# Optimization experiments

Hardware: AMD Instinct MI355X
Metric: run time of the kernel (lower is better)

## Reference

```python
import jax, jax.numpy as jnp
import numpy as np
import math

B, T, N, D = 8, 12, 1000, 256
H, R = 8, 32
HD = D // H
E = 4 * D  # SwiGLU expansion


def setup_inputs() -> dict:
    key = jax.random.key(0)
    ks = jax.random.split(key, 12)
    s = 0.02
    return {
        "x": jax.random.normal(ks[0], (B, T, N, D), jnp.float32),
        "z": jax.random.normal(ks[1], (B, T, N, D), jnp.float32),
        # block params
        "norm1_w": jnp.ones((D,), jnp.float32),
        "norm2_w": jnp.ones((D,), jnp.float32),
        "alpha": jnp.float32(math.log(9)),
        "beta": jnp.float32(math.log(math.sqrt(2) + 1)),
        "gamma": jnp.float32(math.log(9)),
        "delta": jnp.float32(math.log(math.sqrt(2) + 1)),
        # low-rank attention params (Linear stored as [in, out])
        "Wq": jax.random.normal(ks[2], (D, D), jnp.float32) * s,
        "bq": jnp.zeros((D,), jnp.float32),
        "key_param": jax.random.normal(ks[3], (R, H, HD), jnp.float32),
        "Wv": jax.random.normal(ks[4], (D, D), jnp.float32) * s,
        "bv": jnp.zeros((D,), jnp.float32),
        "mha_alpha": jnp.full((H, 1), math.log(9), jnp.float32),
        "mha_beta": jnp.full((H, 1), math.log(0.01), jnp.float32),
        # SwiGLU FFN params
        "W1": jax.random.normal(ks[5], (D, E), jnp.float32) * s,
        "b1": jnp.zeros((E,), jnp.float32),
        "W2": jax.random.normal(ks[6], (D, E), jnp.float32) * s,
        "b2": jnp.zeros((E,), jnp.float32),
        "W3": jax.random.normal(ks[7], (E, D), jnp.float32) * s,
        "b3": jnp.zeros((D,), jnp.float32),
    }


def _rms_norm(x, w, eps=1e-6):
    return w * (x * jax.lax.rsqrt(jnp.mean(x * x, axis=-1, keepdims=True) + eps))


def reference(x, z, norm1_w, norm2_w, alpha, beta, gamma, delta,
              Wq, bq, key_param, Wv, bv, mha_alpha, mha_beta,
              W1, b1, W2, b2, W3, b3):
    sig = jax.nn.sigmoid
    x1 = _rms_norm(x, norm1_w)
    z1 = _rms_norm(sig(gamma) * x1 + sig(delta) * z, norm2_w)

    # SwiGLU FFN (dropout is identity in eval)
    ffn = (jax.nn.silu(x1 @ W1 + b1) * (x1 @ W2 + b2)) @ W3 + b3

    # Low-rank spatial attention
    q = (z1 @ Wq + bq).reshape(B, T, N, H, HD)
    attn = jnp.einsum('btnhd,rhd->btnhr', q, key_param) / jnp.float32(HD) ** 0.5
    xv = (x1 @ Wv + bv).reshape(B, T, N, H, HD)
    v = jnp.einsum('btnhr,btnhd->btrhd', jax.nn.softmax(attn, axis=-1), xv)
    v = jnp.einsum('btnhr,btrhd->btnhd', jax.nn.softmax(attn, axis=2), v)
    v = sig(mha_alpha) * xv + sig(mha_beta) * v  # (H,1) broadcasts over (h,d)
    mha = v.reshape(B, T, N, D)

    return sig(alpha) * ffn + sig(beta) * mha
```

## Files before the change

### kernel.cpp

```cpp
#include <hip/hip_runtime.h>
#include <math.h>

#define MT 96000
#define DD 256
#define EE 1024
#define NBT 96
#define NSEQ 1000

typedef __attribute__((ext_vector_type(8))) short bf16x8;
typedef __attribute__((ext_vector_type(4))) short bf16x4;
typedef __attribute__((ext_vector_type(4))) float f32x4;

__device__ __forceinline__ short f2b(float f) {
  union { float f; unsigned u; } v; v.f = f;
  unsigned r = (v.u + 0x7FFFu + ((v.u >> 16) & 1u)) >> 16;
  return (short)r;
}
__device__ __forceinline__ float b2f(short s) {
  union { unsigned u; float f; } v; v.u = ((unsigned)(unsigned short)s) << 16;
  return v.f;
}
__device__ __forceinline__ float sigf(float x) { return 1.f / (1.f + __expf(-x)); }
__device__ __forceinline__ f32x4 mfma16(bf16x8 a, bf16x8 b, f32x4 c) {
  return __builtin_amdgcn_mfma_f32_16x16x32_bf16(a, b, c, 0, 0, 0);
}
__device__ __forceinline__ unsigned cvtpk(float lo, float hi) {
  unsigned r;
  asm("v_cvt_pk_bf16_f32 %0, %1, %2" : "=v"(r) : "v"(lo), "v"(hi));
  return r;
}
__device__ __forceinline__ void gl_lds16(const short* gp, short* lp) {
  __builtin_amdgcn_global_load_lds(
      (const __attribute__((address_space(1))) void*)gp,
      (__attribute__((address_space(3))) void*)lp, 16, 0, 0);
}

__global__ __launch_bounds__(256) void k_prep(
    const float* __restrict__ Wq, const float* __restrict__ bq,
    const float* __restrict__ key, const float* __restrict__ Wv,
    const float* __restrict__ W1, const float* __restrict__ W2,
    const float* __restrict__ W3,
    short* __restrict__ W1t, short* __restrict__ W2t, short* __restrict__ W3t,
    short* __restrict__ Wvt, short* __restrict__ Wqkt, float* __restrict__ bqk)
{
  int i = blockIdx.x * 256 + threadIdx.x;
  { int e = i >> 8, c = i & 255;
    W1t[i] = f2b(W1[c * EE + e]);
    W2t[i] = f2b(W2[c * EE + e]); }
  { int n = i >> 10, e = i & 1023;
    W3t[i] = f2b(W3[e * DD + n]); }
  if (i < 65536) {
    int n = i >> 8, c = i & 255;
    Wvt[i] = f2b(Wv[c * DD + n]);
    int h = n >> 5, r = n & 31;
    float acc = 0.f;
    for (int d = 0; d < 32; ++d)
      acc += Wq[c * DD + h * 32 + d] * key[(r * 8 + h) * 32 + d];
    Wqkt[i] = f2b(acc * 0.17677669529663687f);
  }
  if (i < 256) {
    int h = i >> 5, r = i & 31;
    float acc = 0.f;
    for (int d = 0; d < 32; ++d)
      acc += bq[h * 32 + d] * key[(r * 8 + h) * 32 + d];
    bqk[i] = acc * 0.17677669529663687f;
  }
}

__global__ __launch_bounds__(256) void k_norm(
    const float* __restrict__ x, const float* __restrict__ z,
    const float* __restrict__ nw1, const float* __restrict__ nw2,
    const float* __restrict__ gamma, const float* __restrict__ delta,
    short* __restrict__ x1bp, short* __restrict__ z1bp)
{
  int tok = blockIdx.x * 4 + (threadIdx.x >> 6);
  int lane = threadIdx.x & 63;
  size_t rbase = (size_t)tok * DD;
  float4 xv = ((const float4*)(x + rbase))[lane];
  float ss = xv.x*xv.x + xv.y*xv.y + xv.z*xv.z + xv.w*xv.w;
  #pragma unroll
  for (int mm = 1; mm < 64; mm <<= 1) ss += __shfl_xor(ss, mm);
  float inv = rsqrtf(ss * 0.00390625f + 1e-6f);
  float4 wv = ((const float4*)nw1)[lane];
  float xa = xv.x * inv * wv.x, xb = xv.y * inv * wv.y,
        xc = xv.z * inv * wv.z, xd = xv.w * inv * wv.w;
  bf16x4 xo = { f2b(xa), f2b(xb), f2b(xc), f2b(xd) };
  ((bf16x4*)(x1bp + rbase))[lane] = xo;
  float sg = sigf(gamma[0]), sd = sigf(delta[0]);
  float4 zv = ((const float4*)(z + rbase))[lane];
  float t0 = sg*xa + sd*zv.x, t1 = sg*xb + sd*zv.y,
        t2 = sg*xc + sd*zv.z, t3 = sg*xd + sd*zv.w;
  float s2 = t0*t0 + t1*t1 + t2*t2 + t3*t3;
  #pragma unroll
  for (int mm = 1; mm < 64; mm <<= 1) s2 += __shfl_xor(s2, mm);
  float inv2 = rsqrtf(s2 * 0.00390625f + 1e-6f);
  float4 w2v = ((const float4*)nw2)[lane];
  bf16x4 zo = { f2b(t0*inv2*w2v.x), f2b(t1*inv2*w2v.y),
                f2b(t2*inv2*w2v.z), f2b(t3*inv2*w2v.w) };
  ((bf16x4*)(z1bp + rbase))[lane] = zo;
}

__global__ __launch_bounds__(256) void k_gemm256(
    const short* __restrict__ A, const short* __restrict__ Bt,
    const float* __restrict__ bias, short* __restrict__ C)
{
  __shared__ __align__(16) short As[64 * 40];
  __shared__ __align__(16) short Bs[64 * 40];
  int row0 = blockIdx.x * 64, col0 = blockIdx.y * 64;
  int tid = threadIdx.x, lane = tid & 63, w = tid >> 6;
  int mh = (w & 1) * 32, nh = (w >> 1) * 32;
  int l15 = lane & 15, ko = (lane >> 4) * 8;
  int lrow = tid >> 2, lch = (tid & 3) * 8;
  f32x4 acc[2][2] = {};
  for (int k0 = 0; k0 < 256; k0 += 32) {
    *(bf16x8*)&As[lrow * 40 + lch] = *(const bf16x8*)&A[(row0 + lrow) * 256 + k0 + lch];
    *(bf16x8*)&Bs[lrow * 40 + lch] = *(const bf16x8*)&Bt[(col0 + lrow) * 256 + k0 + lch];
    __syncthreads();
    bf16x8 af[2], bfr[2];
    #pragma unroll
    for (int t = 0; t < 2; ++t) {
      af[t]  = *(const bf16x8*)&As[(mh + t * 16 + l15) * 40 + ko];
      bfr[t] = *(const bf16x8*)&Bs[(nh + t * 16 + l15) * 40 + ko];
    }
    #pragma unroll
    for (int tm = 0; tm < 2; ++tm)
      #pragma unroll
      for (int tn = 0; tn < 2; ++tn)
        acc[tm][tn] = mfma16(af[tm], bfr[tn], acc[tm][tn]);
    __syncthreads();
  }
  #pragma unroll
  for (int tm = 0; tm < 2; ++tm)
    #pragma unroll
    for (int tn = 0; tn < 2; ++tn) {
      int n = col0 + nh + tn * 16 + l15;
      float bv = bias[n];
      #pragma unroll
      for (int r = 0; r < 4; ++r) {
        int m = row0 + mh + tm * 16 + (lane >> 4) * 4 + r;
        C[m * 256 + n] = f2b(acc[tm][tn][r] + bv);
      }
    }
}

__global__ __launch_bounds__(256, 2) void k_ffn(
    const short* __restrict__ x1bp,
    const short* __restrict__ W1t, const short* __restrict__ W2t,
    const short* __restrict__ W3t,
    const float* __restrict__ b1, const float* __restrict__ b2,
    const float* __restrict__ b3, const float* __restrict__ alpha,
    float* __restrict__ out)
{
  __shared__ __align__(16) short As[64 * 256];
  __shared__ __align__(16) short Hs[64 * 72];
  __shared__ __align__(16) short WR[4 * 4096];
  __shared__ __align__(16) short Bb[2048];
  int row0 = blockIdx.x * 64;
  int tid = threadIdx.x, lane = tid & 63, w = tid >> 6;
  int l15 = lane & 15, g = lane >> 4;
  int swz = l15 & 7;
  int w16 = w * 16;
  int wb = w * 4096;
  int lr = lane >> 2;
  int lc = (((lane & 3) ^ ((lane >> 3) & 3)) * 8);
  int rsw = (l15 >> 1) & 3;

  #pragma unroll
  for (int it = 0; it < 8; ++it) {
    int idx = it * 256 + tid;
    int rw = idx >> 5, c = idx & 31;
    bf16x8 v = __builtin_nontemporal_load(
        (const bf16x8*)&x1bp[(size_t)(row0 + rw) * 256 + c * 8]);
    *(bf16x8*)&As[rw * 256 + ((c ^ (rw & 7)) * 8)] = v;
  }
  {
    float4 v1 = ((const float4*)b1)[tid];
    float4 v2 = ((const float4*)b2)[tid];
    bf16x4 p1 = { f2b(v1.x), f2b(v1.y), f2b(v1.z), f2b(v1.w) };
    bf16x4 p2 = { f2b(v2.x), f2b(v2.y), f2b(v2.z), f2b(v2.w) };
    *(bf16x4*)&Bb[tid * 4] = p1;
    *(bf16x4*)&Bb[1024 + tid * 4] = p2;
  }
  f32x4 oacc[4][4];
  #pragma unroll
  for (int tn = 0; tn < 4; ++tn) {
    float bb = b3[w * 64 + tn * 16 + l15];
    #pragma unroll
    for (int tm = 0; tm < 4; ++tm) oacc[tm][tn] = (f32x4){bb, bb, bb, bb};
  }
  __syncthreads();

  #pragma unroll
  for (int s = 0; s < 4; ++s) {
    gl_lds16(W1t + (size_t)(w16 + lr) * 256 + s * 32 + lc, &WR[wb + s * 1024]);
    gl_lds16(W2t + (size_t)(w16 + lr) * 256 + s * 32 + lc, &WR[wb + s * 1024 + 512]);
  }

  for (int ec = 0; ec < 16; ++ec) {
    int e0 = ec * 64;
    int e0n = ((ec + 1) & 15) * 64;
    int ew = e0 + w16;
    bf16x4 c1b = *(const bf16x4*)&Bb[ew + g * 4];
    bf16x4 c2b = *(const bf16x4*)&Bb[1024 + ew + g * 4];
    f32x4 i1 = { b2f(c1b[0]), b2f(c1b[1]), b2f(c1b[2]), b2f(c1b[3]) };
    f32x4 i2 = { b2f(c2b[0]), b2f(c2b[1]), b2f(c2b[2]), b2f(c2b[3]) };
    f32x4 h1[4], h2[4];
    #pragma unroll
    for (int tm = 0; tm < 4; ++tm) { h1[tm] = i1; h2[tm] = i2; }
    #pragma unroll
    for (int kk = 0; kk < 8; ++kk) {
      int slot = kk & 3;
      asm volatile("s_waitcnt vmcnt(6)" ::: "memory");
      bf16x8 w1f = *(const bf16x8*)&WR[wb + slot * 1024 + l15 * 32 + ((0 ^ rsw) * 8)
                                       + ((g ^ rsw) * 8) - ((0 ^ rsw) * 8)];
      bf16x8 w2f = *(const bf16x8*)&WR[wb + slot * 1024 + 512 + l15 * 32 + ((g ^ rsw) * 8)];
      int ac = ((kk * 4 + g) ^ swz) * 8;
      bf16x8 a0 = *(const bf16x8*)&As[(l15) * 256 + ac];
      bf16x8 a1 = *(const bf16x8*)&As[(16 + l15) * 256 + ac];
      bf16x8 a2 = *(const bf16x8*)&As[(32 + l15) * 256 + ac];
      bf16x8 a3 = *(const bf16x8*)&As[(48 + l15) * 256 + ac];
      asm volatile("s_waitcnt lgkmcnt(0)" ::: "memory");
      if (kk < 4) {
        gl_lds16(W1t + (size_t)(ew + lr) * 256 + (kk + 4) * 32 + lc,
                 &WR[wb + slot * 1024]);
        gl_lds16(W2t + (size_t)(ew + lr) * 256 + (kk + 4) * 32 + lc,
                 &WR[wb + slot * 1024 + 512]);
      } else {
        int k2i = (kk - 4) >> 1, nh = kk & 1;
        const short* g3 = W3t + (size_t)(w * 64 + nh * 32 + lr) * 1024
                          + e0 + k2i * 32 + lc;
        gl_lds16(g3, &WR[wb + slot * 1024]);
        gl_lds16(g3 + 16 * 1024, &WR[wb + slot * 1024 + 512]);
      }
      h1[0] = mfma16(w1f, a0, h1[0]); h2[0] = mfma16(w2f, a0, h2[0]);
      h1[1] = mfma16(w1f, a1, h1[1]); h2[1] = mfma16(w2f, a1, h2[1]);
      h1[2] = mfma16(w1f, a2, h1[2]); h2[2] = mfma16(w2f, a2, h2[2]);
      h1[3] = mfma16(w1f, a3, h1[3]); h2[3] = mfma16(w2f, a3, h2[3]);
    }
    #pragma unroll
    for (int tm = 0; tm < 4; ++tm) {
      int m = tm * 16 + l15;
      float a0 = h1[tm][0], a1 = h1[tm][1], a2 = h1[tm][2], a3 = h1[tm][3];
      float v0 = a0 * h2[tm][0] * sigf(a0);
      float v1 = a1 * h2[tm][1] * sigf(a1);
      float v2 = a2 * h2[tm][2] * sigf(a2);
      float v3 = a3 * h2[tm][3] * sigf(a3);
      uint2 pk;
      pk.x = cvtpk(v0, v1);
      pk.y = cvtpk(v2, v3);
      *(uint2*)&Hs[m * 72 + w16 + g * 4] = pk;
    }
    asm volatile("s_waitcnt lgkmcnt(0)" ::: "memory");
    __builtin_amdgcn_sched_barrier(0);
    __builtin_amdgcn_s_barrier();
    __builtin_amdgcn_sched_barrier(0);
    #pragma unroll
    for (int k2 = 0; k2 < 2; ++k2) {
      asm volatile("s_waitcnt vmcnt(4)" ::: "memory");
      bf16x8 hf[4];
      #pragma unroll
      for (int tm = 0; tm < 4; ++tm)
        hf[tm] = *(const bf16x8*)&Hs[(tm * 16 + l15) * 72 + k2 * 32 + g * 8];
      bf16x8 w3f[4];
      #pragma unroll
      for (int tn = 0; tn < 4; ++tn)
        w3f[tn] = *(const bf16x8*)&WR[wb + (k2 * 2 + (tn >> 1)) * 1024
                                     + (tn & 1) * 512 + l15 * 32 + ((g ^ rsw) * 8)];
      asm volatile("s_waitcnt lgkmcnt(0)" ::: "memory");
      gl_lds16(W1t + (size_t)(e0n + w16 + lr) * 256 + (k2 * 2) * 32 + lc,
               &WR[wb + (k2 * 2) * 1024]);
      gl_lds16(W2t + (size_t)(e0n + w16 + lr) * 256 + (k2 * 2) * 32 + lc,
               &WR[wb + (k2 * 2) * 1024 + 512]);
      gl_lds16(W1t + (size_t)(e0n + w16 + lr) * 256 + (k2 * 2 + 1) * 32 + lc,
               &WR[wb + (k2 * 2 + 1) * 1024]);
      gl_lds16(W2t + (size_t)(e0n + w16 + lr) * 256 + (k2 * 2 + 1) * 32 + lc,
               &WR[wb + (k2 * 2 + 1) * 1024 + 512]);
      #pragma unroll
      for (int tn = 0; tn < 4; ++tn)
        #pragma unroll
        for (int tm = 0; tm < 4; ++tm)
          oacc[tm][tn] = mfma16(hf[tm], w3f[tn], oacc[tm][tn]);
    }
    __builtin_amdgcn_sched_barrier(0);
    __builtin_amdgcn_s_barrier();
    __builtin_amdgcn_sched_barrier(0);
  }
  asm volatile("s_waitcnt vmcnt(0)" ::: "memory");
  float sa = sigf(alpha[0]);
  #pragma unroll
  for (int tn = 0; tn < 4; ++tn) {
    int n = w * 64 + tn * 16 + l15;
    #pragma unroll
    for (int tm = 0; tm < 4; ++tm)
      #pragma unroll
      for (int r = 0; r < 4; ++r) {
        int m = row0 + tm * 16 + g * 4 + r;
        __builtin_nontemporal_store(sa * oacc[tm][tn][r], &out[(size_t)m * 256 + n]);
      }
  }
}

__global__ __launch_bounds__(256) void k_attn1(
    const short* __restrict__ attnb, const short* __restrict__ xvb,
    float* __restrict__ v1buf, float* __restrict__ colmax, float* __restrict__ colsum)
{
  __shared__ float xr[8][32];
  __shared__ float red[8][32][32];
  __shared__ float mred[8][32], sred[8][32];
  int gid = blockIdx.x;
  int bt = gid >> 3, h = gid & 7;
  int tid = threadIdx.x, r = tid & 31, nl = tid >> 5;
  int base = bt * NSEQ;
  float accd[32];
  #pragma unroll
  for (int d = 0; d < 32; ++d) accd[d] = 0.f;
  float mrun = -1e30f, srun = 0.f;
  for (int it = 0; it < 125; ++it) {
    int tok = base + it * 8 + nl;
    float a = b2f(attnb[(size_t)tok * 256 + h * 32 + r]);
    float rmax = a;
    #pragma unroll
    for (int mm = 16; mm > 0; mm >>= 1) rmax = fmaxf(rmax, __shfl_xor(rmax, mm));
    float ea = __expf(a - rmax);
    float rsum = ea;
    #pragma unroll
    for (int mm = 16; mm > 0; mm >>= 1) rsum += __shfl_xor(rsum, mm);
    float p1 = ea / rsum;
    float nm = fmaxf(mrun, a);
    srun = srun * __expf(mrun - nm) + __expf(a - nm);
    mrun = nm;
    xr[nl][r] = b2f(xvb[(size_t)tok * 256 + h * 32 + r]);
    #pragma unroll
    for (int d = 0; d < 32; ++d) accd[d] += p1 * xr[nl][d];
  }
  #pragma unroll
  for (int d = 0; d < 32; ++d) red[nl][r][d] = accd[d];
  mred[nl][r] = mrun; sred[nl][r] = srun;
  __syncthreads();
  for (int s = 4; s > 0; s >>= 1) {
    if (nl < s)
      #pragma unroll
      for (int d = 0; d < 32; ++d) red[nl][r][d] += red[nl + s][r][d];
    __syncthreads();
  }
  if (nl == 0) {
    for (int d = 0; d < 32; ++d) v1buf[gid * 1024 + r * 32 + d] = red[0][r][d];
    float Mv = -1e30f;
    for (int j = 0; j < 8; ++j) Mv = fmaxf(Mv, mred[j][r]);
    float Sv = 0.f;
    for (int j = 0; j < 8; ++j) Sv += sred[j][r] * __expf(mred[j][r] - Mv);
    colmax[gid * 32 + r] = Mv;
    colsum[gid * 32 + r] = Sv;
  }
}

__global__ __launch_bounds__(256) void k_attn2(
    const short* __restrict__ attnb, const short* __restrict__ xvb,
    const float* __restrict__ v1buf, const float* __restrict__ colmax,
    const float* __restrict__ colsum, const float* __restrict__ mha_alpha,
    const float* __restrict__ mha_beta, const float* __restrict__ beta,
    float* __restrict__ out)
{
  __shared__ float v1s[8 * 1024];
  __shared__ float p2s[256];
  int bt = blockIdx.x, chunk = blockIdx.y;
  int tid = threadIdx.x;
  #pragma unroll
  for (int q = 0; q < 8; ++q)
    ((float4*)v1s)[q * 256 + tid] = ((const float4*)(v1buf + (size_t)bt * 8192))[q * 256 + tid];
  int h = tid >> 5, d = tid & 31;
  float cm  = colmax[bt * 256 + tid];
  float rcs = 1.f / colsum[bt * 256 + tid];
  float sa = sigf(mha_alpha[h]), sb = sigf(mha_beta[h]);
  float sbeta = sigf(beta[0]);
  __syncthreads();
  const float* v1p = v1s + h * 1024 + d;
  int tok0 = bt * NSEQ + chunk * 100;
  for (int tl = 0; tl < 100; ++tl) {
    int tok = tok0 + tl;
    float a = b2f(attnb[(size_t)tok * 256 + tid]);
    p2s[tid] = __expf(a - cm) * rcs;
    float xvv = b2f(xvb[(size_t)tok * 256 + tid]);
    float v2 = 0.f;
    #pragma unroll
    for (int rr = 0; rr < 32; ++rr)
      v2 += p2s[h * 32 + rr] * v1p[rr * 32];
    out[(size_t)tok * 256 + tid] += sbeta * (sa * xvv + sb * v2);
  }
}

extern "C" void kernel_launch(void* const* d_in, const int* in_sizes, int n_in,
                              void* d_out, int out_size, void* d_ws, size_t ws_size,
                              hipStream_t stream) {
  const float* x        = (const float*)d_in[0];
  const float* z        = (const float*)d_in[1];
  const float* norm1_w  = (const float*)d_in[2];
  const float* norm2_w  = (const float*)d_in[3];
  const float* alpha    = (const float*)d_in[4];
  const float* beta     = (const float*)d_in[5];
  const float* gamma    = (const float*)d_in[6];
  const float* delta    = (const float*)d_in[7];
  const float* Wq       = (const float*)d_in[8];
  const float* bq       = (const float*)d_in[9];
  const float* key      = (const float*)d_in[10];
  const float* Wv       = (const float*)d_in[11];
  const float* bv       = (const float*)d_in[12];
  const float* mha_a    = (const float*)d_in[13];
  const float* mha_b    = (const float*)d_in[14];
  const float* W1       = (const float*)d_in[15];
  const float* b1       = (const float*)d_in[16];
  const float* W2       = (const float*)d_in[17];
  const float* b2       = (const float*)d_in[18];
  const float* W3       = (const float*)d_in[19];
  const float* b3       = (const float*)d_in[20];
  float* out = (float*)d_out;
  char* ws = (char*)d_ws;

  short* x1b   = (short*)(ws);
  short* z1b   = (short*)(ws + 49152000);
  short* xvb   = (short*)(ws + 98304000);
  short* attnb = (short*)(ws + 147456000);
  short* W1t   = (short*)(ws + 196608000);
  short* W2t   = (short*)(ws + 197132288);
  short* W3t   = (short*)(ws + 197656576);
  short* Wvt   = (short*)(ws + 198180864);
  short* Wqkt  = (short*)(ws + 198311936);
  float* bqk   = (float*)(ws + 198443008);
  float* v1buf = (float*)(ws + 198444032);
  float* colmax= (float*)(ws + 201589760);
  float* colsum= (float*)(ws + 201688064);

  hipLaunchKernelGGL(k_prep, dim3(1024), dim3(256), 0, stream,
                     Wq, bq, key, Wv, W1, W2, W3, W1t, W2t, W3t, Wvt, Wqkt, bqk);
  hipLaunchKernelGGL(k_norm, dim3(MT / 4), dim3(256), 0, stream,
                     x, z, norm1_w, norm2_w, gamma, delta, x1b, z1b);
  hipLaunchKernelGGL(k_gemm256, dim3(MT / 64, 4), dim3(256), 0, stream,
                     z1b, Wqkt, bqk, attnb);
  hipLaunchKernelGGL(k_gemm256, dim3(MT / 64, 4), dim3(256), 0, stream,
                     x1b, Wvt, bv, xvb);
  hipLaunchKernelGGL(k_ffn, dim3(MT / 64), dim3(256), 0, stream,
                     x1b, W1t, W2t, W3t, b1, b2, b3, alpha, out);
  hipLaunchKernelGGL(k_attn1, dim3(NBT * 8), dim3(256), 0, stream,
                     attnb, xvb, v1buf, colmax, colsum);
  hipLaunchKernelGGL(k_attn2, dim3(NBT, 10), dim3(256), 0, stream,
                     attnb, xvb, v1buf, colmax, colsum, mha_a, mha_b, beta, out);
}
```

Before: 729.3 us.

## Compute full-N GEMM tiles per block, keep v1 in registers, use fast reciprocal

The two 256-wide projection GEMMs now have each block stage a 64x256 A tile in LDS once and compute all 256 output columns, reading weight fragments straight from global memory (L2-resident). The old version reloaded A four times across column blocks and synchronised at every k-step. In attn2, the per-head v1 values are held in 32 registers per thread instead of an 8192-float LDS copy, which cuts LDS traffic and allocation. attn1 replaces a division with a hardware reciprocal, and a redundant index expression in the FFN is simplified. The trade-offs are more register pressure and uncoalesced global weight loads in the GEMM.

```diff
diff --git a/kernel.cpp b/kernel.cpp
--- a/kernel.cpp
+++ b/kernel.cpp
@@ -27,6 +27,11 @@
 __device__ __forceinline__ unsigned cvtpk(float lo, float hi) {
   unsigned r;
   asm("v_cvt_pk_bf16_f32 %0, %1, %2" : "=v"(r) : "v"(lo), "v"(hi));
+  return r;
+}
+__device__ __forceinline__ float frcp(float x) {
+  float r;
+  asm("v_rcp_f32 %0, %1" : "=v"(r) : "v"(x));
   return r;
 }
 __device__ __forceinline__ void gl_lds16(const short* gp, short* lp) {
@@ -100,47 +105,54 @@
   ((bf16x4*)(z1bp + rbase))[lane] = zo;
 }
 
-__global__ __launch_bounds__(256) void k_gemm256(
+__global__ __launch_bounds__(256) void k_gemm_fullN(
     const short* __restrict__ A, const short* __restrict__ Bt,
     const float* __restrict__ bias, short* __restrict__ C)
 {
-  __shared__ __align__(16) short As[64 * 40];
-  __shared__ __align__(16) short Bs[64 * 40];
-  int row0 = blockIdx.x * 64, col0 = blockIdx.y * 64;
+  __shared__ __align__(16) short As[64 * 264];
+  int row0 = blockIdx.x * 64;
   int tid = threadIdx.x, lane = tid & 63, w = tid >> 6;
-  int mh = (w & 1) * 32, nh = (w >> 1) * 32;
-  int l15 = lane & 15, ko = (lane >> 4) * 8;
-  int lrow = tid >> 2, lch = (tid & 3) * 8;
-  f32x4 acc[2][2] = {};
-  for (int k0 = 0; k0 < 256; k0 += 32) {
-    *(bf16x8*)&As[lrow * 40 + lch] = *(const bf16x8*)&A[(row0 + lrow) * 256 + k0 + lch];
-    *(bf16x8*)&Bs[lrow * 40 + lch] = *(const bf16x8*)&Bt[(col0 + lrow) * 256 + k0 + lch];
-    __syncthreads();
-    bf16x8 af[2], bfr[2];
-    #pragma unroll
-    for (int t = 0; t < 2; ++t) {
-      af[t]  = *(const bf16x8*)&As[(mh + t * 16 + l15) * 40 + ko];
-      bfr[t] = *(const bf16x8*)&Bs[(nh + t * 16 + l15) * 40 + ko];
-    }
-    #pragma unroll
-    for (int tm = 0; tm < 2; ++tm)
-      #pragma unroll
-      for (int tn = 0; tn < 2; ++tn)
-        acc[tm][tn] = mfma16(af[tm], bfr[tn], acc[tm][tn]);
-    __syncthreads();
-  }
-  #pragma unroll
-  for (int tm = 0; tm < 2; ++tm)
-    #pragma unroll
-    for (int tn = 0; tn < 2; ++tn) {
-      int n = col0 + nh + tn * 16 + l15;
-      float bv = bias[n];
+  int l15 = lane & 15, g = lane >> 4;
+  #pragma unroll
+  for (int it = 0; it < 8; ++it) {
+    int idx = it * 256 + tid;
+    int rw = idx >> 5, ch = (idx & 31) * 8;
+    *(bf16x8*)&As[rw * 264 + ch] = *(const bf16x8*)&A[(size_t)(row0 + rw) * 256 + ch];
+  }
+  f32x4 acc[4][4];
+  #pragma unroll
+  for (int tn = 0; tn < 4; ++tn) {
+    float bb = bias[w * 64 + tn * 16 + l15];
+    #pragma unroll
+    for (int tm = 0; tm < 4; ++tm) acc[tm][tn] = (f32x4){bb, bb, bb, bb};
+  }
+  __syncthreads();
+  #pragma unroll
+  for (int kk = 0; kk < 8; ++kk) {
+    bf16x8 af[4], wf[4];
+    #pragma unroll
+    for (int tm = 0; tm < 4; ++tm)
+      af[tm] = *(const bf16x8*)&As[(tm * 16 + l15) * 264 + kk * 32 + g * 8];
+    #pragma unroll
+    for (int tn = 0; tn < 4; ++tn)
+      wf[tn] = *(const bf16x8*)&Bt[(size_t)(w * 64 + tn * 16 + l15) * 256 + kk * 32 + g * 8];
+    #pragma unroll
+    for (int tn = 0; tn < 4; ++tn)
+      #pragma unroll
+      for (int tm = 0; tm < 4; ++tm)
+        acc[tm][tn] = mfma16(af[tm], wf[tn], acc[tm][tn]);
+  }
+  #pragma unroll
+  for (int tn = 0; tn < 4; ++tn) {
+    int n = w * 64 + tn * 16 + l15;
+    #pragma unroll
+    for (int tm = 0; tm < 4; ++tm)
       #pragma unroll
       for (int r = 0; r < 4; ++r) {
-        int m = row0 + mh + tm * 16 + (lane >> 4) * 4 + r;
-        C[m * 256 + n] = f2b(acc[tm][tn][r] + bv);
+        int m = row0 + tm * 16 + g * 4 + r;
+        C[(size_t)m * 256 + n] = f2b(acc[tm][tn][r]);
       }
-    }
+  }
 }
 
 __global__ __launch_bounds__(256, 2) void k_ffn(
@@ -211,8 +223,7 @@
     for (int kk = 0; kk < 8; ++kk) {
       int slot = kk & 3;
       asm volatile("s_waitcnt vmcnt(6)" ::: "memory");
-      bf16x8 w1f = *(const bf16x8*)&WR[wb + slot * 1024 + l15 * 32 + ((0 ^ rsw) * 8)
-                                       + ((g ^ rsw) * 8) - ((0 ^ rsw) * 8)];
+      bf16x8 w1f = *(const bf16x8*)&WR[wb + slot * 1024 + l15 * 32 + ((g ^ rsw) * 8)];
       bf16x8 w2f = *(const bf16x8*)&WR[wb + slot * 1024 + 512 + l15 * 32 + ((g ^ rsw) * 8)];
       int ac = ((kk * 4 + g) ^ swz) * 8;
       bf16x8 a0 = *(const bf16x8*)&As[(l15) * 256 + ac];
@@ -325,7 +336,7 @@
     float rsum = ea;
     #pragma unroll
     for (int mm = 16; mm > 0; mm >>= 1) rsum += __shfl_xor(rsum, mm);
-    float p1 = ea / rsum;
+    float p1 = ea * frcp(rsum);
     float nm = fmaxf(mrun, a);
     srun = srun * __expf(mrun - nm) + __expf(a - nm);
     mrun = nm;
@@ -361,20 +372,18 @@
     const float* __restrict__ mha_beta, const float* __restrict__ beta,
     float* __restrict__ out)
 {
-  __shared__ float v1s[8 * 1024];
   __shared__ float p2s[256];
   int bt = blockIdx.x, chunk = blockIdx.y;
   int tid = threadIdx.x;
-  #pragma unroll
-  for (int q = 0; q < 8; ++q)
-    ((float4*)v1s)[q * 256 + tid] = ((const float4*)(v1buf + (size_t)bt * 8192))[q * 256 + tid];
   int h = tid >> 5, d = tid & 31;
+  float v1reg[32];
+  #pragma unroll
+  for (int rr = 0; rr < 32; ++rr)
+    v1reg[rr] = v1buf[(size_t)bt * 8192 + h * 1024 + rr * 32 + d];
   float cm  = colmax[bt * 256 + tid];
   float rcs = 1.f / colsum[bt * 256 + tid];
   float sa = sigf(mha_alpha[h]), sb = sigf(mha_beta[h]);
   float sbeta = sigf(beta[0]);
-  __syncthreads();
-  const float* v1p = v1s + h * 1024 + d;
   int tok0 = bt * NSEQ + chunk * 100;
   for (int tl = 0; tl < 100; ++tl) {
     int tok = tok0 + tl;
@@ -384,7 +393,7 @@
     float v2 = 0.f;
     #pragma unroll
     for (int rr = 0; rr < 32; ++rr)
-      v2 += p2s[h * 32 + rr] * v1p[rr * 32];
+      v2 += p2s[h * 32 + rr] * v1reg[rr];
     out[(size_t)tok * 256 + tid] += sbeta * (sa * xvv + sb * v2);
   }
 }
@@ -434,9 +443,9 @@
                      Wq, bq, key, Wv, W1, W2, W3, W1t, W2t, W3t, Wvt, Wqkt, bqk);
   hipLaunchKernelGGL(k_norm, dim3(MT / 4), dim3(256), 0, stream,
                      x, z, norm1_w, norm2_w, gamma, delta, x1b, z1b);
-  hipLaunchKernelGGL(k_gemm256, dim3(MT / 64, 4), dim3(256), 0, stream,
+  hipLaunchKernelGGL(k_gemm_fullN, dim3(MT / 64), dim3(256), 0, stream,
                      z1b, Wqkt, bqk, attnb);
-  hipLaunchKernelGGL(k_gemm256, dim3(MT / 64, 4), dim3(256), 0, stream,
+  hipLaunchKernelGGL(k_gemm_fullN, dim3(MT / 64), dim3(256), 0, stream,
                      x1b, Wvt, bv, xvb);
   hipLaunchKernelGGL(k_ffn, dim3(MT / 64), dim3(256), 0, stream,
                      x1b, W1t, W2t, W3t, b1, b2, b3, alpha, out);
```

After: 726.8 us. No clear change (-0.3%).
